# Kernel optimization log

Measured on AMD Instinct MI355X. Metric: run time of the kernel, lower is better.

## Reference

```python
import jax, jax.numpy as jnp
import numpy as np

B, NQ, NK, C, H = 4, 1024, 1024, 768, 12
DH = C // H
SCALE = DH ** -0.5
EPS = 1e-5  # nn.LayerNorm default
NEG_INF = float('-inf')


def _ln(x, g, b):
    m = jnp.mean(x, axis=-1, keepdims=True)
    v = jnp.mean((x - m) ** 2, axis=-1, keepdims=True)
    return (x - m) * jax.lax.rsqrt(v + EPS) * g + b


def _heads(t):  # [B,N,C] -> [B,H,N,Dh]
    Bq, N, _ = t.shape
    return t.reshape(Bq, N, H, DH).transpose(0, 2, 1, 3)


def setup_inputs() -> dict:
    key = jax.random.key(0)
    ks = jax.random.split(key, 32)
    w = lambda k, shape: jax.random.normal(k, shape, jnp.float32) * 0.02
    g = lambda k: 1.0 + jax.random.normal(k, (C,), jnp.float32) * 0.02
    b = lambda k: jax.random.normal(k, (C,), jnp.float32) * 0.02
    inp = {
        'x': jax.random.normal(ks[0], (B, NQ, C), jnp.float32),
        'y': jax.random.normal(ks[1], (B, NK, C), jnp.float32),
        'xpos': jnp.arange(B * NQ, dtype=jnp.int32).reshape(B, NQ),
        'ypos': jnp.arange(B * NK, dtype=jnp.int32).reshape(B, NK),
        'mask': jax.random.randint(ks[2], (NQ, NK), 0, 2) > 0,
        'similarities': jax.random.normal(ks[3], (B, H, NQ, NK), jnp.float32),
        # norms
        'ln1_g': g(ks[4]), 'ln1_b': b(ks[5]),
        'ln2_g': g(ks[6]), 'ln2_b': b(ks[7]),
        'ln3_g': g(ks[8]), 'ln3_b': b(ks[9]),
        'lny_g': g(ks[10]), 'lny_b': b(ks[11]),
        # self-attn (qkv_bias=False)
        'qkv_w': w(ks[12], (3 * C, C)),
        'aproj_w': w(ks[13], (C, C)), 'aproj_b': b(ks[14]),
        # cross-attn
        'pq_w': w(ks[15], (C, C)), 'pk_w': w(ks[16], (C, C)), 'pv_w': w(ks[17], (C, C)),
        'cproj_w': w(ks[18], (C, C)), 'cproj_b': b(ks[19]),
        # mlp (hidden = 4*C)
        'fc1_w': w(ks[20], (4 * C, C)), 'fc1_b': jax.random.normal(ks[21], (4 * C,), jnp.float32) * 0.02,
        'fc2_w': w(ks[22], (C, 4 * C)), 'fc2_b': b(ks[23]),
    }
    return inp


def reference(x, y, xpos, ypos, mask, similarities,
              ln1_g, ln1_b, ln2_g, ln2_b, ln3_g, ln3_b, lny_g, lny_b,
              qkv_w, aproj_w, aproj_b,
              pq_w, pk_w, pv_w, cproj_w, cproj_b,
              fc1_w, fc1_b, fc2_w, fc2_b):
    # ---- self-attention (rope=None, dropout=0) ----
    xn = _ln(x, ln1_g, ln1_b)
    qkv = (xn @ qkv_w.T).reshape(B, NQ, 3, H, DH).transpose(2, 0, 3, 1, 4)
    q, k, v = qkv[0], qkv[1], qkv[2]                       # [B,H,Nq,Dh]
    attn = jax.nn.softmax(jnp.einsum('bhqd,bhkd->bhqk', q, k) * SCALE, axis=-1)
    sa = jnp.einsum('bhqk,bhkd->bhqd', attn, v).transpose(0, 2, 1, 3).reshape(B, NQ, C)
    x = x + sa @ aproj_w.T + aproj_b

    # ---- sparse cross-attention with similarity bias + mask ----
    y_ = _ln(y, lny_g, lny_b)
    xn2 = _ln(x, ln2_g, ln2_b)
    cq = _heads(xn2 @ pq_w.T)                              # [B,H,Nq,Dh]
    ck = _heads(y_ @ pk_w.T)                               # [B,H,Nk,Dh]
    cv = _heads(y_ @ pv_w.T)
    scores = jnp.einsum('bhqd,bhkd->bhqk', cq, ck) * SCALE
    sims_c = similarities - jnp.mean(similarities, axis=1, keepdims=True)
    scores = scores + sims_c
    scores = jnp.where(mask[None, None], scores, NEG_INF)
    cattn = jax.nn.softmax(scores, axis=-1)
    ca = jnp.einsum('bhqk,bhkd->bhqd', cattn, cv).transpose(0, 2, 1, 3).reshape(B, NQ, C)
    x = x + ca @ cproj_w.T + cproj_b

    # ---- MLP (exact GELU, as nn.GELU default) ----
    xn3 = _ln(x, ln3_g, ln3_b)
    h = jax.nn.gelu(xn3 @ fc1_w.T + fc1_b, approximate=False)
    x = x + h @ fc2_w.T + fc2_b
    return (x, y)
```

## Files before the change

### kernel.cpp

```cpp
#include <hip/hip_runtime.h>
#include <cstdint>
#include <cstddef>


typedef __bf16 bf16;
typedef __attribute__((ext_vector_type(8))) __bf16 bf16x8;
typedef __attribute__((ext_vector_type(4))) __bf16 bf16x4;
typedef __attribute__((ext_vector_type(4))) float f32x4;

typedef __attribute__((address_space(1))) void gvoid;
typedef __attribute__((address_space(3))) void lvoid;

#define DEVI static __device__ __forceinline__

DEVI void gload16(const void* g, void* l) {
  __builtin_amdgcn_global_load_lds((gvoid*)(uintptr_t)g, (lvoid*)(uintptr_t)l, 16, 0, 0);
}

DEVI f32x4 mfma_bf16(bf16x8 a, bf16x8 b, f32x4 c) {
  return __builtin_amdgcn_mfma_f32_16x16x32_bf16(a, b, c, 0, 0, 0);
}


template<int BM, int BN, bool BIAS, bool GELU, bool RES, bool OBF, bool VT>
DEVI void gemm_dev(bf16* As, bf16* Bs, int by, int bx,
                   const bf16* __restrict__ A, const bf16* __restrict__ Bt,
                   const float* __restrict__ bias, const float* __restrict__ res,
                   bf16* __restrict__ Cb, float* __restrict__ Cf,
                   bf16* __restrict__ vtOut, int vtBase, int N, int K)
{
  constexpr int WM = BM / 2, WN = BN / 2;
  constexpr int FM = WM / 16, FN = WN / 16;
  const int tid = threadIdx.x;
  const int lane = tid & 63;
  const int wv = tid >> 6;
  const int wr = wv >> 1, wc = wv & 1;
  const int l15 = lane & 15, lg = lane >> 4;
  const int bm = by * BM, bn = bx * BN;

  f32x4 acc[FM][FN];
  const f32x4 z = {0.f, 0.f, 0.f, 0.f};
  #pragma unroll
  for (int i = 0; i < FM; ++i)
    #pragma unroll
    for (int jj = 0; jj < FN; ++jj) acc[i][jj] = z;

  for (int k0 = 0; k0 < K; k0 += 64) {
    __syncthreads();
    #pragma unroll
    for (int c = tid; c < BM * 8; c += 256) {
      const int row = c >> 3, colb = (c & 7) << 4;
      gload16((const char*)A + ((size_t)(bm + row) * K + k0) * 2 + colb,
              (char*)As + (size_t)c * 16);
    }
    #pragma unroll
    for (int c = tid; c < BN * 8; c += 256) {
      const int row = c >> 3, colb = (c & 7) << 4;
      gload16((const char*)Bt + ((size_t)(bn + row) * K + k0) * 2 + colb,
              (char*)Bs + (size_t)c * 16);
    }
    __syncthreads();
    #pragma unroll
    for (int kk = 0; kk < 64; kk += 32) {
      bf16x8 af[FM], bfr[FN];
      #pragma unroll
      for (int mi = 0; mi < FM; ++mi)
        af[mi] = *(const bf16x8*)(As + (size_t)(wr * WM + mi * 16 + l15) * 64 + kk + lg * 8);
      #pragma unroll
      for (int ni = 0; ni < FN; ++ni)
        bfr[ni] = *(const bf16x8*)(Bs + (size_t)(wc * WN + ni * 16 + l15) * 64 + kk + lg * 8);
      #pragma unroll
      for (int mi = 0; mi < FM; ++mi)
        #pragma unroll
        for (int ni = 0; ni < FN; ++ni)
          acc[mi][ni] = mfma_bf16(af[mi], bfr[ni], acc[mi][ni]);
    }
  }

  #pragma unroll
  for (int mi = 0; mi < FM; ++mi) {
    const int row0 = bm + wr * WM + mi * 16 + lg * 4;
    #pragma unroll
    for (int ni = 0; ni < FN; ++ni) {
      const int col = bn + wc * WN + ni * 16 + l15;
      if constexpr (VT) {
        if (col >= vtBase) {
          const int hd = col - vtBase;
          const int bb = row0 >> 10, n0 = row0 & 1023;
          bf16x4 ov;
          #pragma unroll
          for (int r = 0; r < 4; ++r) ov[r] = (bf16)acc[mi][ni][r];
          *(bf16x4*)(vtOut + ((size_t)(bb * 768 + hd)) * 1024 + n0) = ov;
          continue;
        }
      }
      #pragma unroll
      for (int r = 0; r < 4; ++r) {
        float v = acc[mi][ni][r];
        if constexpr (BIAS) v += bias[col];
        if constexpr (GELU) v = 0.5f * v * (1.0f + erff(v * 0.70710678118654752f));
        if constexpr (RES)  v += res[(size_t)(row0 + r) * N + col];
        if constexpr (OBF)  Cb[(size_t)(row0 + r) * N + col] = (bf16)v;
        else                Cf[(size_t)(row0 + r) * N + col] = v;
      }
    }
  }
}

DEVI void lnw_dev(int row,
                  const float* __restrict__ xin, const float* __restrict__ g,
                  const float* __restrict__ be, bf16* __restrict__ out)
{
  const int lane = threadIdx.x & 63;
  const f32x4* xr = (const f32x4*)(xin + (size_t)row * 768);
  f32x4 v[3];
  #pragma unroll
  for (int j = 0; j < 3; ++j) v[j] = xr[lane + 64 * j];
  float s = 0.f;
  #pragma unroll
  for (int j = 0; j < 3; ++j) s += v[j][0] + v[j][1] + v[j][2] + v[j][3];
  #pragma unroll
  for (int o = 32; o; o >>= 1) s += __shfl_xor(s, o);
  const float mean = s * (1.0f / 768.0f);
  float q = 0.f;
  #pragma unroll
  for (int j = 0; j < 3; ++j)
    #pragma unroll
    for (int e = 0; e < 4; ++e) { const float d = v[j][e] - mean; q += d * d; }
  #pragma unroll
  for (int o = 32; o; o >>= 1) q += __shfl_xor(q, o);
  const float inv = rsqrtf(q * (1.0f / 768.0f) + 1e-5f);
  #pragma unroll
  for (int j = 0; j < 3; ++j) {
    const int c = lane + 64 * j;
    const f32x4 gv = ((const f32x4*)g)[c];
    const f32x4 bv = ((const f32x4*)be)[c];
    bf16x4 o4;
    #pragma unroll
    for (int e = 0; e < 4; ++e)
      o4[e] = (bf16)((v[j][e] - mean) * inv * gv[e] + bv[e]);
    *((bf16x4*)out + (size_t)row * 192 + c) = o4;
  }
}


struct CvtArgs {
  const float* src[8];
  bf16* dst[8];
  int end[8];
};

__global__ __launch_bounds__(256)
void prep_k(CvtArgs a,
            const float* __restrict__ x, const float* __restrict__ g1,
            const float* __restrict__ b1, bf16* __restrict__ xn,
            const float* __restrict__ y, const float* __restrict__ gy,
            const float* __restrict__ by_, bf16* __restrict__ yln)
{
  const int f = blockIdx.x;
  const int t = threadIdx.x;
  if (f < 2304) {
    #pragma unroll
    for (int j = 0; j < 4; ++j) {
      const int i = f * 1024 + j * 256 + t;
      int s = 0;
      #pragma unroll
      for (int k = 0; k < 7; ++k) s += (i >= a.end[k]) ? 1 : 0;
      const int base = s ? a.end[s - 1] : 0;
      const int off = i - base;
      const f32x4 v = *((const f32x4*)a.src[s] + off);
      bf16x4 o;
      o[0] = (bf16)v[0]; o[1] = (bf16)v[1]; o[2] = (bf16)v[2]; o[3] = (bf16)v[3];
      *(bf16x4*)(a.dst[s] + (size_t)off * 4) = o;
    }
  } else {
    const int row = (f - 2304) * 4 + (t >> 6);
    if (row < 4096) lnw_dev(row, x, g1, b1, xn);
    else            lnw_dev(row - 4096, y, gy, by_, yln);
  }
}

__global__ __launch_bounds__(256)
void bias_k(const float* __restrict__ sim,
            const unsigned char* __restrict__ mask,
            bf16* __restrict__ biasOut)
{
  __shared__ float S[12 * 1032];
  __shared__ int red[4];
  const int blk = blockIdx.x;
  const int b = blk >> 10, q = blk & 1023;
  const int t = threadIdx.x, lane = t & 63, w = t >> 6;

  int ds = mask[t * 4 + 1] + mask[t * 4 + 2] + mask[t * 4 + 3];
  #pragma unroll
  for (int o = 32; o; o >>= 1) ds += __shfl_xor(ds, o);
  if (lane == 0) red[w] = ds;

  const float* sb = sim + (size_t)b * 12 * 1048576;
  #pragma unroll
  for (int i = 0; i < 3; ++i) {
    const int h = w + i * 4;
    const f32x4* src = (const f32x4*)(sb + ((size_t)h * 1024 + q) * 1024);
    #pragma unroll
    for (int jj = 0; jj < 4; ++jj) {
      const int c = lane + 64 * jj;
      *(f32x4*)(&S[h * 1032 + c * 4]) = src[c];
    }
  }
  __syncthreads();
  const int msh = ((red[0] + red[1] + red[2] + red[3]) == 0) ? 2 : 0;

  const int k4 = t * 4;
  float mb[4];
  if (msh == 0) {
    const uchar4 mv = *(const uchar4*)(mask + (size_t)q * 1024 + k4);
    mb[0] = mv.x ? 0.f : -1e30f; mb[1] = mv.y ? 0.f : -1e30f;
    mb[2] = mv.z ? 0.f : -1e30f; mb[3] = mv.w ? 0.f : -1e30f;
  } else {
    const int4 mv = *(const int4*)((const int*)mask + (size_t)q * 1024 + k4);
    mb[0] = mv.x ? 0.f : -1e30f; mb[1] = mv.y ? 0.f : -1e30f;
    mb[2] = mv.z ? 0.f : -1e30f; mb[3] = mv.w ? 0.f : -1e30f;
  }

  f32x4 acc = {0.f, 0.f, 0.f, 0.f};
  #pragma unroll
  for (int h = 0; h < 12; ++h) acc += *(const f32x4*)(&S[h * 1032 + k4]);
  const f32x4 mean = acc * (1.0f / 12.0f);

  bf16* ob = biasOut + (size_t)(b * 1024 + q) * 12 * 1024;
  #pragma unroll
  for (int h = 0; h < 12; ++h) {
    const f32x4 sv = *(const f32x4*)(&S[h * 1032 + k4]);
    bf16x4 o;
    #pragma unroll
    for (int j = 0; j < 4; ++j)
      o[j] = (bf16)(sv[j] - mean[j] + mb[j]);
    *(bf16x4*)(ob + h * 1024 + k4) = o;
  }
}

__global__ __launch_bounds__(256)
void apkv_k(const bf16* __restrict__ sa, const bf16* __restrict__ w_ap,
            const float* __restrict__ apb, const float* __restrict__ x,
            float* __restrict__ x1,
            const bf16* __restrict__ yln, const bf16* __restrict__ w_pkv,
            bf16* __restrict__ ckv, bf16* __restrict__ cvtT)
{
  __shared__ bf16 As[128 * 64];
  __shared__ bf16 Bs[128 * 64];
  const int f = blockIdx.x;
  if (f < 384) {
    const int xcd = f & 7, j = f >> 3;
    const int by = xcd + 8 * (j % 8);
    const int bx = j / 8;
    gemm_dev<64,128,true,false,true,false,false>(As, Bs, by, bx,
        sa, w_ap, apb, x, nullptr, x1, nullptr, 0, 768, 768);
  } else {
    const int g = f - 384;
    const int xcd = g & 7, j = g >> 3;
    const int by = xcd + 8 * (j % 4);
    const int bx = j / 4;
    gemm_dev<128,128,false,false,false,true,true>(As, Bs, by, bx,
        yln, w_pkv, nullptr, nullptr, ckv, nullptr, cvtT, 768, 1536, 768);
  }
}

__global__ __launch_bounds__(256)
void fc2copy_k(const bf16* __restrict__ hbuf, const bf16* __restrict__ w_f2,
               const float* __restrict__ f2b, const float* __restrict__ x2,
               float* __restrict__ outp,
               const float* __restrict__ y, float* __restrict__ ycopy)
{
  __shared__ bf16 As[128 * 64];
  __shared__ bf16 Bs[128 * 64];
  const int f = blockIdx.x;
  if (f < 384) {
    const int xcd = f & 7, j = f >> 3;
    const int by = xcd + 8 * (j % 8);
    const int bx = j / 8;
    gemm_dev<64,128,true,false,true,false,false>(As, Bs, by, bx,
        hbuf, w_f2, f2b, x2, nullptr, outp, nullptr, 0, 768, 3072);
  } else {
    for (int i = (f - 384) * 256 + threadIdx.x; i < 786432; i += 512 * 256)
      ((f32x4*)ycopy)[i] = ((const f32x4*)y)[i];
  }
}

template<int BM, int BN, bool BIAS, bool GELU, bool RES, bool OBF, bool VT>
__global__ __launch_bounds__(256)
void gemm_bt(const bf16* __restrict__ A, const bf16* __restrict__ Bt,
             const float* __restrict__ bias, const float* __restrict__ res,
             bf16* __restrict__ Cb, float* __restrict__ Cf,
             bf16* __restrict__ vtOut, int vtBase,
             int nyPerXcd, int N, int K)
{
  __shared__ bf16 As[BM * 64];
  __shared__ bf16 Bs[BN * 64];
  const int f = blockIdx.x;
  const int xcd = f & 7, j = f >> 3;
  const int by = xcd + 8 * (j % nyPerXcd);
  const int bx = j / nyPerXcd;
  gemm_dev<BM,BN,BIAS,GELU,RES,OBF,VT>(As, Bs, by, bx,
      A, Bt, bias, res, Cb, Cf, vtOut, vtBase, N, K);
}

__global__ __launch_bounds__(256)
void ln_k(const float* __restrict__ xin, const float* __restrict__ g,
          const float* __restrict__ be, bf16* __restrict__ out)
{
  lnw_dev(blockIdx.x * 4 + (threadIdx.x >> 6), xin, g, be, out);
}

template<int CROSS>
__global__ __launch_bounds__(256, 3)
void fattn_k(const bf16* __restrict__ Qp, int ldq,
             const bf16* __restrict__ Kp, int ldk,
             const bf16* __restrict__ Vt,
             const bf16* __restrict__ bias,
             bf16* __restrict__ Out)
{
  __shared__ bf16 Kl[2][64 * 64];
  __shared__ bf16 Vl[2][64 * 64];
  __shared__ bf16 Pl[4][16 * 72];

  const int f = blockIdx.x;
  const int r8 = f & 7, rest = f >> 3;
  const int c6 = rest % 6, qt = rest / 6;
  const int pp = r8 + 8 * c6;
  const int b = pp / 12, hh = pp % 12;
  const int tid = threadIdx.x, lane = tid & 63, wq = tid >> 6;
  const int l15 = lane & 15, lg = lane >> 4;

  bf16x8 qreg0, qreg1;
  {
    const bf16* qsrc = Qp + (size_t)(b * 1024 + qt * 64 + wq * 16 + l15) * ldq + hh * 64 + lg * 8;
    qreg0 = *(const bf16x8*)qsrc;
    qreg1 = *(const bf16x8*)(qsrc + 32);
  }
  const char* Kbase = (const char*)(Kp + (size_t)b * 1024 * ldk + hh * 64);
  const char* Vbase = (const char*)(Vt + (size_t)(b * 12 + hh) * 64 * 1024);
  const bf16* biasRow = nullptr;
  if constexpr (CROSS)
    biasRow = bias + ((size_t)(b * 1024 + qt * 64 + wq * 16 + l15) * 12 + hh) * 1024;

  f32x4 oacc[4];
  const f32x4 z = {0.f, 0.f, 0.f, 0.f};
  #pragma unroll
  for (int i = 0; i < 4; ++i) oacc[i] = z;
  float m_run = -1e30f, l_run = 0.f;

  char* PlW = (char*)&Pl[wq][0];
  const int swz = (l15 & 7) << 4;

  auto stage = [&](int buf, int t) {
    const int k0 = t * 64;
    #pragma unroll
    for (int jj = 0; jj < 2; ++jj) {
      const int c = jj * 256 + tid;
      const int r = c >> 3;
      const int sw = ((c & 7) ^ (r & 7)) << 4;
      gload16(Kbase + ((size_t)(k0 + r) * ldk) * 2 + sw, (char*)&Kl[buf][0] + (size_t)c * 16);
      gload16(Vbase + (size_t)r * 2048 + (size_t)k0 * 2 + sw, (char*)&Vl[buf][0] + (size_t)c * 16);
    }
  };

  stage(0, 0);
  __syncthreads();

  for (int t = 0; t < 16; ++t) {
    const int cur = t & 1;
    const int k0 = t * 64;
    if (t < 15) stage(cur ^ 1, t + 1);

    bf16x4 bv[4];
    if constexpr (CROSS) {
      const bf16* bp = biasRow + k0 + lg * 4;
      #pragma unroll
      for (int ni = 0; ni < 4; ++ni) bv[ni] = *(const bf16x4*)(bp + ni * 16);
    }

    f32x4 sacc[4];
    #pragma unroll
    for (int i = 0; i < 4; ++i) sacc[i] = z;
    #pragma unroll
    for (int ni = 0; ni < 4; ++ni) {
      const int rowb = (ni * 16 + l15) * 128;
      const bf16x8 a0 = *(const bf16x8*)((char*)&Kl[cur][0] + rowb + ((lg * 16) ^ swz));
      const bf16x8 a1 = *(const bf16x8*)((char*)&Kl[cur][0] + rowb + ((64 + lg * 16) ^ swz));
      sacc[ni] = mfma_bf16(a0, qreg0, sacc[ni]);
      sacc[ni] = mfma_bf16(a1, qreg1, sacc[ni]);
    }

    float sv[16];
    #pragma unroll
    for (int ni = 0; ni < 4; ++ni)
      #pragma unroll
      for (int r = 0; r < 4; ++r)
        sv[ni * 4 + r] = sacc[ni][r] * 0.125f;
    if constexpr (CROSS) {
      #pragma unroll
      for (int ni = 0; ni < 4; ++ni)
        #pragma unroll
        for (int r = 0; r < 4; ++r)
          sv[ni * 4 + r] += (float)bv[ni][r];
    }
    float mx = sv[0];
    #pragma unroll
    for (int jj = 1; jj < 16; ++jj) mx = fmaxf(mx, sv[jj]);
    mx = fmaxf(mx, __shfl_xor(mx, 16));
    mx = fmaxf(mx, __shfl_xor(mx, 32));
    const float mnew = fmaxf(m_run, mx);
    const float corr = __expf(m_run - mnew);
    m_run = mnew;
    float ps = 0.f;
    #pragma unroll
    for (int jj = 0; jj < 16; ++jj) { sv[jj] = __expf(sv[jj] - mnew); ps += sv[jj]; }
    l_run = l_run * corr + ps;

    #pragma unroll
    for (int ni = 0; ni < 4; ++ni) {
      bf16x4 pw;
      #pragma unroll
      for (int r = 0; r < 4; ++r) pw[r] = (bf16)sv[ni * 4 + r];
      *(bf16x4*)(PlW + l15 * 144 + ni * 32 + lg * 8) = pw;
    }
    float cr[4];
    #pragma unroll
    for (int r = 0; r < 4; ++r) cr[r] = __shfl(corr, ((lane >> 4) << 2) + r);
    #pragma unroll
    for (int nd = 0; nd < 4; ++nd)
      #pragma unroll
      for (int r = 0; r < 4; ++r) oacc[nd][r] *= cr[r];

    const bf16x8 p0 = *(const bf16x8*)(PlW + l15 * 144 + lg * 16);
    const bf16x8 p1 = *(const bf16x8*)(PlW + l15 * 144 + 64 + lg * 16);
    #pragma unroll
    for (int nd = 0; nd < 4; ++nd) {
      const int rowb = (nd * 16 + l15) * 128;
      const bf16x8 v0 = *(const bf16x8*)((char*)&Vl[cur][0] + rowb + ((lg * 16) ^ swz));
      const bf16x8 v1 = *(const bf16x8*)((char*)&Vl[cur][0] + rowb + ((64 + lg * 16) ^ swz));
      oacc[nd] = mfma_bf16(p0, v0, oacc[nd]);
      oacc[nd] = mfma_bf16(p1, v1, oacc[nd]);
    }
    __syncthreads();
  }

  float ls = l_run + __shfl_xor(l_run, 16);
  ls += __shfl_xor(ls, 32);
  const float inv = 1.0f / ls;
  float ivr[4];
  #pragma unroll
  for (int r = 0; r < 4; ++r) ivr[r] = __shfl(inv, ((lane >> 4) << 2) + r);
  bf16* ob = Out + (size_t)(b * 1024 + qt * 64 + wq * 16 + lg * 4) * 768 + hh * 64 + l15;
  #pragma unroll
  for (int r = 0; r < 4; ++r)
    #pragma unroll
    for (int nd = 0; nd < 4; ++nd)
      ob[(size_t)r * 768 + nd * 16] = (bf16)(oacc[nd][r] * ivr[r]);
}

extern "C" void kernel_launch(void* const* d_in, const int* in_sizes, int n_in,
                              void* d_out, int out_size, void* d_ws, size_t ws_size,
                              hipStream_t stream)
{
  (void)in_sizes; (void)n_in; (void)out_size; (void)ws_size;
  const float* x    = (const float*)d_in[0];
  const float* y    = (const float*)d_in[1];
  const unsigned char* mask = (const unsigned char*)d_in[4];
  const float* sim  = (const float*)d_in[5];
  const float* ln1g = (const float*)d_in[6];
  const float* ln1b = (const float*)d_in[7];
  const float* ln2g = (const float*)d_in[8];
  const float* ln2b = (const float*)d_in[9];
  const float* ln3g = (const float*)d_in[10];
  const float* ln3b = (const float*)d_in[11];
  const float* lnyg = (const float*)d_in[12];
  const float* lnyb = (const float*)d_in[13];
  const float* qkvw = (const float*)d_in[14];
  const float* apw  = (const float*)d_in[15];
  const float* apb  = (const float*)d_in[16];
  const float* pqw  = (const float*)d_in[17];
  const float* pkw  = (const float*)d_in[18];
  const float* pvw  = (const float*)d_in[19];
  const float* cpw  = (const float*)d_in[20];
  const float* cpb  = (const float*)d_in[21];
  const float* f1w  = (const float*)d_in[22];
  const float* f1b  = (const float*)d_in[23];
  const float* f2w  = (const float*)d_in[24];
  const float* f2b  = (const float*)d_in[25];

  char* ws = (char*)d_ws;
  size_t off = 0;
  auto alloc = [&](size_t bytes) -> void* {
    off = (off + 255) & ~(size_t)255;
    void* p = ws + off;
    off += bytes;
    return p;
  };
  const size_t T = 4096;
  bf16* w_qkv = (bf16*)alloc((size_t)2304 * 768 * 2);
  bf16* w_ap  = (bf16*)alloc((size_t)768 * 768 * 2);
  bf16* w_pq  = (bf16*)alloc((size_t)768 * 768 * 2);
  bf16* w_pkv = (bf16*)alloc((size_t)1536 * 768 * 2);
  bf16* w_cp  = (bf16*)alloc((size_t)768 * 768 * 2);
  bf16* w_f1  = (bf16*)alloc((size_t)3072 * 768 * 2);
  bf16* w_f2  = (bf16*)alloc((size_t)768 * 3072 * 2);
  bf16* xn    = (bf16*)alloc(T * 768 * 2);
  bf16* qkvo  = (bf16*)alloc(T * 2304 * 2);
  bf16* vt    = (bf16*)alloc((size_t)48 * 64 * 1024 * 2);
  bf16* sa    = (bf16*)alloc(T * 768 * 2);
  float* x1   = (float*)alloc(T * 768 * 4);
  bf16* yln   = (bf16*)alloc(T * 768 * 2);
  bf16* xn2   = (bf16*)alloc(T * 768 * 2);
  bf16* cqf   = (bf16*)alloc(T * 768 * 2);
  bf16* ckv   = (bf16*)alloc(T * 1536 * 2);
  bf16* cvtT  = (bf16*)alloc((size_t)48 * 64 * 1024 * 2);
  bf16* biasA = (bf16*)alloc((size_t)4 * 1024 * 12 * 1024 * 2);
  bf16* ca    = (bf16*)alloc(T * 768 * 2);
  float* x2   = (float*)alloc(T * 768 * 4);
  bf16* xn3   = (bf16*)alloc(T * 768 * 2);
  bf16* hbuf  = (bf16*)alloc(T * 3072 * 2);

  CvtArgs a;
  {
    const float* srcs[8] = {qkvw, apw, pqw, pkw, pvw, cpw, f1w, f2w};
    bf16* dsts[8] = {w_qkv, w_ap, w_pq, w_pkv, w_pkv + 768 * 768, w_cp, w_f1, w_f2};
    const int n4s[8] = {442368, 147456, 147456, 147456, 147456, 147456, 589824, 589824};
    int cum = 0;
    for (int j = 0; j < 8; ++j) {
      a.src[j] = srcs[j]; a.dst[j] = dsts[j];
      cum += n4s[j]; a.end[j] = cum;
    }
  }

  prep_k<<<4352, 256, 0, stream>>>(a, x, ln1g, ln1b, xn, y, lnyg, lnyb, yln);

  bias_k<<<4096, 256, 0, stream>>>(sim, mask, biasA);

  gemm_bt<128,128,false,false,false,true,true><<<576, 256, 0, stream>>>(
      xn, w_qkv, nullptr, nullptr, qkvo, nullptr, vt, 1536, 4, 2304, 768);

  fattn_k<0><<<768, 256, 0, stream>>>(
      qkvo, 2304, qkvo + 768, 2304, vt, nullptr, sa);

  apkv_k<<<768, 256, 0, stream>>>(sa, w_ap, apb, x, x1, yln, w_pkv, ckv, cvtT);

  ln_k<<<1024, 256, 0, stream>>>(x1, ln2g, ln2b, xn2);

  gemm_bt<64,128,false,false,false,true,false><<<384, 256, 0, stream>>>(
      xn2, w_pq, nullptr, nullptr, cqf, nullptr, nullptr, 0, 8, 768, 768);

  fattn_k<1><<<768, 256, 0, stream>>>(
      cqf, 768, ckv, 1536, cvtT, biasA, ca);

  gemm_bt<64,128,true,false,true,false,false><<<384, 256, 0, stream>>>(
      ca, w_cp, cpb, x1, nullptr, x2, nullptr, 0, 8, 768, 768);

  ln_k<<<1024, 256, 0, stream>>>(x2, ln3g, ln3b, xn3);

  gemm_bt<128,128,true,true,false,true,false><<<768, 256, 0, stream>>>(
      xn3, w_f1, f1b, nullptr, hbuf, nullptr, nullptr, 0, 4, 3072, 768);

  fc2copy_k<<<896, 256, 0, stream>>>(
      hbuf, w_f2, f2b, x2, (float*)d_out, y, (float*)d_out + 3145728);
}
```

Measured before the change: 388.0 us.

## Split similarity-bias kernel into chunks co-scheduled with earlier GEMM/attention kernels

Removes the standalone bias_k launch and spreads its 4096 row-blocks across four earlier kernels (QKV GEMM, self-attention, apkv, pq GEMM) as extra trailing blocks, so this memory-bound work can overlap with compute-bound work. The per-row bias routine is also rewritten to keep the 12 head values in registers instead of staging them in shared memory, which removes the LDS round trip and the barrier. The cost is extra register pressure in the fused kernels and possible interference with GEMM/attention block scheduling and occupancy.

New measurement: 349.9 us. 9.8% less time.

```diff
diff --git a/kernel.cpp b/kernel.cpp
--- a/kernel.cpp
+++ b/kernel.cpp
@@ -107,110 +107,35 @@
   }
 }
 
-DEVI void lnw_dev(int row,
-                  const float* __restrict__ xin, const float* __restrict__ g,
-                  const float* __restrict__ be, bf16* __restrict__ out)
-{
-  const int lane = threadIdx.x & 63;
-  const f32x4* xr = (const f32x4*)(xin + (size_t)row * 768);
-  f32x4 v[3];
-  #pragma unroll
-  for (int j = 0; j < 3; ++j) v[j] = xr[lane + 64 * j];
-  float s = 0.f;
-  #pragma unroll
-  for (int j = 0; j < 3; ++j) s += v[j][0] + v[j][1] + v[j][2] + v[j][3];
-  #pragma unroll
-  for (int o = 32; o; o >>= 1) s += __shfl_xor(s, o);
-  const float mean = s * (1.0f / 768.0f);
-  float q = 0.f;
-  #pragma unroll
-  for (int j = 0; j < 3; ++j)
-    #pragma unroll
-    for (int e = 0; e < 4; ++e) { const float d = v[j][e] - mean; q += d * d; }
-  #pragma unroll
-  for (int o = 32; o; o >>= 1) q += __shfl_xor(q, o);
-  const float inv = rsqrtf(q * (1.0f / 768.0f) + 1e-5f);
-  #pragma unroll
-  for (int j = 0; j < 3; ++j) {
-    const int c = lane + 64 * j;
-    const f32x4 gv = ((const f32x4*)g)[c];
-    const f32x4 bv = ((const f32x4*)be)[c];
-    bf16x4 o4;
-    #pragma unroll
-    for (int e = 0; e < 4; ++e)
-      o4[e] = (bf16)((v[j][e] - mean) * inv * gv[e] + bv[e]);
-    *((bf16x4*)out + (size_t)row * 192 + c) = o4;
-  }
-}
-
-
-struct CvtArgs {
-  const float* src[8];
-  bf16* dst[8];
-  int end[8];
-};
-
-__global__ __launch_bounds__(256)
-void prep_k(CvtArgs a,
-            const float* __restrict__ x, const float* __restrict__ g1,
-            const float* __restrict__ b1, bf16* __restrict__ xn,
-            const float* __restrict__ y, const float* __restrict__ gy,
-            const float* __restrict__ by_, bf16* __restrict__ yln)
-{
-  const int f = blockIdx.x;
-  const int t = threadIdx.x;
-  if (f < 2304) {
-    #pragma unroll
-    for (int j = 0; j < 4; ++j) {
-      const int i = f * 1024 + j * 256 + t;
-      int s = 0;
-      #pragma unroll
-      for (int k = 0; k < 7; ++k) s += (i >= a.end[k]) ? 1 : 0;
-      const int base = s ? a.end[s - 1] : 0;
-      const int off = i - base;
-      const f32x4 v = *((const f32x4*)a.src[s] + off);
-      bf16x4 o;
-      o[0] = (bf16)v[0]; o[1] = (bf16)v[1]; o[2] = (bf16)v[2]; o[3] = (bf16)v[3];
-      *(bf16x4*)(a.dst[s] + (size_t)off * 4) = o;
-    }
-  } else {
-    const int row = (f - 2304) * 4 + (t >> 6);
-    if (row < 4096) lnw_dev(row, x, g1, b1, xn);
-    else            lnw_dev(row - 4096, y, gy, by_, yln);
-  }
-}
-
-__global__ __launch_bounds__(256)
-void bias_k(const float* __restrict__ sim,
-            const unsigned char* __restrict__ mask,
-            bf16* __restrict__ biasOut)
-{
-  __shared__ float S[12 * 1032];
-  __shared__ int red[4];
-  const int blk = blockIdx.x;
+DEVI void biasr_dev(int blk,
+                    const float* __restrict__ sim,
+                    const unsigned char* __restrict__ mask,
+                    bf16* __restrict__ out)
+{
   const int b = blk >> 10, q = blk & 1023;
-  const int t = threadIdx.x, lane = t & 63, w = t >> 6;
-
-  int ds = mask[t * 4 + 1] + mask[t * 4 + 2] + mask[t * 4 + 3];
+  const int t = threadIdx.x, lane = t & 63;
+
+  int ds = 0;
+  #pragma unroll
+  for (int i = 0; i < 4; ++i) {
+    const int idx = (lane * 4 + i) * 4;
+    ds += mask[idx + 1] + mask[idx + 2] + mask[idx + 3];
+  }
   #pragma unroll
   for (int o = 32; o; o >>= 1) ds += __shfl_xor(ds, o);
-  if (lane == 0) red[w] = ds;
-
+  const int msh = (ds == 0) ? 2 : 0;
+
+  const int k4 = t * 4;
   const float* sb = sim + (size_t)b * 12 * 1048576;
-  #pragma unroll
-  for (int i = 0; i < 3; ++i) {
-    const int h = w + i * 4;
-    const f32x4* src = (const f32x4*)(sb + ((size_t)h * 1024 + q) * 1024);
-    #pragma unroll
-    for (int jj = 0; jj < 4; ++jj) {
-      const int c = lane + 64 * jj;
-      *(f32x4*)(&S[h * 1032 + c * 4]) = src[c];
-    }
-  }
-  __syncthreads();
-  const int msh = ((red[0] + red[1] + red[2] + red[3]) == 0) ? 2 : 0;
-
-  const int k4 = t * 4;
+  f32x4 sv[12];
+  f32x4 acc = {0.f, 0.f, 0.f, 0.f};
+  #pragma unroll
+  for (int h = 0; h < 12; ++h) {
+    sv[h] = *(const f32x4*)(sb + ((size_t)h * 1024 + q) * 1024 + k4);
+    acc += sv[h];
+  }
+  const f32x4 mean = acc * (1.0f / 12.0f);
+
   float mb[4];
   if (msh == 0) {
     const uchar4 mv = *(const uchar4*)(mask + (size_t)q * 1024 + k4);
@@ -222,21 +147,113 @@
     mb[2] = mv.z ? 0.f : -1e30f; mb[3] = mv.w ? 0.f : -1e30f;
   }
 
-  f32x4 acc = {0.f, 0.f, 0.f, 0.f};
-  #pragma unroll
-  for (int h = 0; h < 12; ++h) acc += *(const f32x4*)(&S[h * 1032 + k4]);
-  const f32x4 mean = acc * (1.0f / 12.0f);
-
-  bf16* ob = biasOut + (size_t)(b * 1024 + q) * 12 * 1024;
+  bf16* ob = out + (size_t)(b * 1024 + q) * 12 * 1024;
   #pragma unroll
   for (int h = 0; h < 12; ++h) {
-    const f32x4 sv = *(const f32x4*)(&S[h * 1032 + k4]);
     bf16x4 o;
     #pragma unroll
     for (int j = 0; j < 4; ++j)
-      o[j] = (bf16)(sv[j] - mean[j] + mb[j]);
+      o[j] = (bf16)(sv[h][j] - mean[j] + mb[j]);
     *(bf16x4*)(ob + h * 1024 + k4) = o;
   }
+}
+
+DEVI void lnw_dev(int row,
+                  const float* __restrict__ xin, const float* __restrict__ g,
+                  const float* __restrict__ be, bf16* __restrict__ out)
+{
+  const int lane = threadIdx.x & 63;
+  const f32x4* xr = (const f32x4*)(xin + (size_t)row * 768);
+  f32x4 v[3];
+  #pragma unroll
+  for (int j = 0; j < 3; ++j) v[j] = xr[lane + 64 * j];
+  float s = 0.f;
+  #pragma unroll
+  for (int j = 0; j < 3; ++j) s += v[j][0] + v[j][1] + v[j][2] + v[j][3];
+  #pragma unroll
+  for (int o = 32; o; o >>= 1) s += __shfl_xor(s, o);
+  const float mean = s * (1.0f / 768.0f);
+  float q = 0.f;
+  #pragma unroll
+  for (int j = 0; j < 3; ++j)
+    #pragma unroll
+    for (int e = 0; e < 4; ++e) { const float d = v[j][e] - mean; q += d * d; }
+  #pragma unroll
+  for (int o = 32; o; o >>= 1) q += __shfl_xor(q, o);
+  const float inv = rsqrtf(q * (1.0f / 768.0f) + 1e-5f);
+  #pragma unroll
+  for (int j = 0; j < 3; ++j) {
+    const int c = lane + 64 * j;
+    const f32x4 gv = ((const f32x4*)g)[c];
+    const f32x4 bv = ((const f32x4*)be)[c];
+    bf16x4 o4;
+    #pragma unroll
+    for (int e = 0; e < 4; ++e)
+      o4[e] = (bf16)((v[j][e] - mean) * inv * gv[e] + bv[e]);
+    *((bf16x4*)out + (size_t)row * 192 + c) = o4;
+  }
+}
+
+
+struct CvtArgs {
+  const float* src[8];
+  bf16* dst[8];
+  int end[8];
+};
+
+__global__ __launch_bounds__(256)
+void prep_k(CvtArgs a,
+            const float* __restrict__ x, const float* __restrict__ g1,
+            const float* __restrict__ b1, bf16* __restrict__ xn,
+            const float* __restrict__ y, const float* __restrict__ gy,
+            const float* __restrict__ by_, bf16* __restrict__ yln)
+{
+  const int f = blockIdx.x;
+  const int t = threadIdx.x;
+  if (f < 2304) {
+    #pragma unroll
+    for (int j = 0; j < 4; ++j) {
+      const int i = f * 1024 + j * 256 + t;
+      int s = 0;
+      #pragma unroll
+      for (int k = 0; k < 7; ++k) s += (i >= a.end[k]) ? 1 : 0;
+      const int base = s ? a.end[s - 1] : 0;
+      const int off = i - base;
+      const f32x4 v = *((const f32x4*)a.src[s] + off);
+      bf16x4 o;
+      o[0] = (bf16)v[0]; o[1] = (bf16)v[1]; o[2] = (bf16)v[2]; o[3] = (bf16)v[3];
+      *(bf16x4*)(a.dst[s] + (size_t)off * 4) = o;
+    }
+  } else {
+    const int row = (f - 2304) * 4 + (t >> 6);
+    if (row < 4096) lnw_dev(row, x, g1, b1, xn);
+    else            lnw_dev(row - 4096, y, gy, by_, yln);
+  }
+}
+
+template<int BM, int BN, bool BIAS, bool GELU, bool RES, bool OBF, bool VT>
+__global__ __launch_bounds__(256)
+void gemm_bt(const bf16* __restrict__ A, const bf16* __restrict__ Bt,
+             const float* __restrict__ bias, const float* __restrict__ res,
+             bf16* __restrict__ Cb, float* __restrict__ Cf,
+             bf16* __restrict__ vtOut, int vtBase,
+             int nyPerXcd, int N, int K,
+             int nCompute,
+             const float* __restrict__ bsim, const unsigned char* __restrict__ bmask,
+             bf16* __restrict__ bout, int bbase)
+{
+  __shared__ bf16 As[BM * 64];
+  __shared__ bf16 Bs[BN * 64];
+  const int f = blockIdx.x;
+  if (f >= nCompute) {
+    biasr_dev(bbase + f - nCompute, bsim, bmask, bout);
+    return;
+  }
+  const int xcd = f & 7, j = f >> 3;
+  const int by = xcd + 8 * (j % nyPerXcd);
+  const int bx = j / nyPerXcd;
+  gemm_dev<BM,BN,BIAS,GELU,RES,OBF,VT>(As, Bs, by, bx,
+      A, Bt, bias, res, Cb, Cf, vtOut, vtBase, N, K);
 }
 
 __global__ __launch_bounds__(256)
@@ -244,11 +261,17 @@
             const float* __restrict__ apb, const float* __restrict__ x,
             float* __restrict__ x1,
             const bf16* __restrict__ yln, const bf16* __restrict__ w_pkv,
-            bf16* __restrict__ ckv, bf16* __restrict__ cvtT)
+            bf16* __restrict__ ckv, bf16* __restrict__ cvtT,
+            const float* __restrict__ bsim, const unsigned char* __restrict__ bmask,
+            bf16* __restrict__ bout, int bbase)
 {
   __shared__ bf16 As[128 * 64];
   __shared__ bf16 Bs[128 * 64];
   const int f = blockIdx.x;
+  if (f >= 768) {
+    biasr_dev(bbase + f - 768, bsim, bmask, bout);
+    return;
+  }
   if (f < 384) {
     const int xcd = f & 7, j = f >> 3;
     const int by = xcd + 8 * (j % 8);
@@ -286,24 +309,6 @@
   }
 }
 
-template<int BM, int BN, bool BIAS, bool GELU, bool RES, bool OBF, bool VT>
-__global__ __launch_bounds__(256)
-void gemm_bt(const bf16* __restrict__ A, const bf16* __restrict__ Bt,
-             const float* __restrict__ bias, const float* __restrict__ res,
-             bf16* __restrict__ Cb, float* __restrict__ Cf,
-             bf16* __restrict__ vtOut, int vtBase,
-             int nyPerXcd, int N, int K)
-{
-  __shared__ bf16 As[BM * 64];
-  __shared__ bf16 Bs[BN * 64];
-  const int f = blockIdx.x;
-  const int xcd = f & 7, j = f >> 3;
-  const int by = xcd + 8 * (j % nyPerXcd);
-  const int bx = j / nyPerXcd;
-  gemm_dev<BM,BN,BIAS,GELU,RES,OBF,VT>(As, Bs, by, bx,
-      A, Bt, bias, res, Cb, Cf, vtOut, vtBase, N, K);
-}
-
 __global__ __launch_bounds__(256)
 void ln_k(const float* __restrict__ xin, const float* __restrict__ g,
           const float* __restrict__ be, bf16* __restrict__ out)
@@ -317,13 +322,20 @@
              const bf16* __restrict__ Kp, int ldk,
              const bf16* __restrict__ Vt,
              const bf16* __restrict__ bias,
-             bf16* __restrict__ Out)
+             bf16* __restrict__ Out,
+             int nCompute,
+             const float* __restrict__ bsim, const unsigned char* __restrict__ bmask,
+             bf16* __restrict__ bout, int bbase)
 {
   __shared__ bf16 Kl[2][64 * 64];
   __shared__ bf16 Vl[2][64 * 64];
   __shared__ bf16 Pl[4][16 * 72];
 
   const int f = blockIdx.x;
+  if (f >= nCompute) {
+    biasr_dev(bbase + f - nCompute, bsim, bmask, bout);
+    return;
+  }
   const int r8 = f & 7, rest = f >> 3;
   const int c6 = rest % 6, qt = rest / 6;
   const int pp = r8 + 8 * c6;
@@ -535,31 +547,36 @@
 
   prep_k<<<4352, 256, 0, stream>>>(a, x, ln1g, ln1b, xn, y, lnyg, lnyb, yln);
 
-  bias_k<<<4096, 256, 0, stream>>>(sim, mask, biasA);
-
-  gemm_bt<128,128,false,false,false,true,true><<<576, 256, 0, stream>>>(
-      xn, w_qkv, nullptr, nullptr, qkvo, nullptr, vt, 1536, 4, 2304, 768);
-
-  fattn_k<0><<<768, 256, 0, stream>>>(
-      qkvo, 2304, qkvo + 768, 2304, vt, nullptr, sa);
-
-  apkv_k<<<768, 256, 0, stream>>>(sa, w_ap, apb, x, x1, yln, w_pkv, ckv, cvtT);
+  gemm_bt<128,128,false,false,false,true,true><<<1600, 256, 0, stream>>>(
+      xn, w_qkv, nullptr, nullptr, qkvo, nullptr, vt, 1536, 4, 2304, 768,
+      576, sim, mask, biasA, 0);
+
+  fattn_k<0><<<1792, 256, 0, stream>>>(
+      qkvo, 2304, qkvo + 768, 2304, vt, nullptr, sa,
+      768, sim, mask, biasA, 1024);
+
+  apkv_k<<<1792, 256, 0, stream>>>(sa, w_ap, apb, x, x1, yln, w_pkv, ckv, cvtT,
+                                   sim, mask, biasA, 2048);
 
   ln_k<<<1024, 256, 0, stream>>>(x1, ln2g, ln2b, xn2);
 
-  gemm_bt<64,128,false,false,false,true,false><<<384, 256, 0, stream>>>(
-      xn2, w_pq, nullptr, nullptr, cqf, nullptr, nullptr, 0, 8, 768, 768);
+  gemm_bt<64,128,false,false,false,true,false><<<1408, 256, 0, stream>>>(
+      xn2, w_pq, nullptr, nullptr, cqf, nullptr, nullptr, 0, 8, 768, 768,
+      384, sim, mask, biasA, 3072);
 
   fattn_k<1><<<768, 256, 0, stream>>>(
-      cqf, 768, ckv, 1536, cvtT, biasA, ca);
+      cqf, 768, ckv, 1536, cvtT, biasA, ca,
+      768, sim, mask, biasA, 0);
 
   gemm_bt<64,128,true,false,true,false,false><<<384, 256, 0, stream>>>(
-      ca, w_cp, cpb, x1, nullptr, x2, nullptr, 0, 8, 768, 768);
+      ca, w_cp, cpb, x1, nullptr, x2, nullptr, 0, 8, 768, 768,
+      384, sim, mask, biasA, 0);
 
   ln_k<<<1024, 256, 0, stream>>>(x2, ln3g, ln3b, xn3);
 
   gemm_bt<128,128,true,true,false,true,false><<<768, 256, 0, stream>>>(
-      xn3, w_f1, f1b, nullptr, hbuf, nullptr, nullptr, 0, 4, 3072, 768);
+      xn3, w_f1, f1b, nullptr, hbuf, nullptr, nullptr, 0, 4, 3072, 768,
+      768, sim, mask, biasA, 0);
 
   fc2copy_k<<<896, 256, 0, stream>>>(
       hbuf, w_f2, f2b, x2, (float*)d_out, y, (float*)d_out + 3145728);
```
